# Kernel optimization log

Hardware: AMD Instinct MI355X
Metric: run time of the kernel (lower is better)

The kernel has to match this reference:

```python
import jax, jax.numpy as jnp
import numpy as np

RANK = 16
BN_EPS = 1e-5


def _head(xf, qw, qb, kw, kb, vw, vb, qlw, klw, ow, ob):
    # xf: [B, S, c]  (c = split channels)
    Q = xf @ qw.T + qb
    K = xf @ kw.T + kb
    V = xf @ vw.T + vb
    Ql = Q @ qlw.T                      # [B, S, rank]
    Kl = K @ klw.T                      # [B, S, rank]
    scores = jnp.einsum('bsr,btr->bst', Ql, Kl) / jnp.sqrt(jnp.float32(RANK))
    attn = jax.nn.softmax(scores, axis=-1)   # [B, S, S]
    out = jnp.einsum('bst,btc->bsc', attn, V)
    return out @ ow.T + ob


def _bn(x, g, b):
    # training-mode BatchNorm2d: biased batch stats over (B, H, W)
    m = x.mean(axis=(0, 2, 3), keepdims=True)
    v = x.var(axis=(0, 2, 3), keepdims=True)
    return (x - m) / jnp.sqrt(v + BN_EPS) * g[None, :, None, None] + b[None, :, None, None]


def reference(x, qw, qb, kw, kb, vw, vb, qlw, klw, ow, ob,
              f1w, f1b, f2w, f2b, g1, b1, g2, b2):
    B, C, H, W = x.shape
    sc = C // 4
    S = H * W
    xf = x.reshape(B, C, S).transpose(0, 2, 1)   # [B, S, C]

    outs = []
    prev = jnp.zeros_like(xf[..., :sc])
    for i in range(4):  # hierarchical: head i consumes split_i + out_{i-1}
        xi = xf[..., i * sc:(i + 1) * sc] + prev
        prev = _head(xi, qw[i], qb[i], kw[i], kb[i], vw[i], vb[i],
                     qlw[i], klw[i], ow[i], ob[i])
        outs.append(prev)

    concat = jnp.concatenate(outs, axis=-1).transpose(0, 2, 1).reshape(B, C, H, W)
    out = x + _bn(concat, g1, b1)

    # FFN: 1x1 conv 256->1024, exact GELU, 1x1 conv 1024->256 (dropout = eval / identity)
    h = jnp.einsum('bchw,oc->bohw', out, f1w) + f1b[None, :, None, None]
    h = jax.nn.gelu(h, approximate=False)
    h = jnp.einsum('bchw,oc->bohw', h, f2w) + f2b[None, :, None, None]
    return out + _bn(h, g2, b2)


def setup_inputs() -> dict:
    key = jax.random.key(0)
    ks = jax.random.split(key, 16)
    B, C, H, W = 2, 256, 64, 64
    sc = C // 4
    s = 0.05
    inp = {
        'x':   jax.random.normal(ks[0], (B, C, H, W), jnp.float32),
        'qw':  jax.random.normal(ks[1], (4, sc, sc), jnp.float32) * s,
        'qb':  jnp.zeros((4, sc), jnp.float32),
        'kw':  jax.random.normal(ks[2], (4, sc, sc), jnp.float32) * s,
        'kb':  jnp.zeros((4, sc), jnp.float32),
        'vw':  jax.random.normal(ks[3], (4, sc, sc), jnp.float32) * s,
        'vb':  jnp.zeros((4, sc), jnp.float32),
        'qlw': jax.random.normal(ks[4], (4, RANK, sc), jnp.float32) * s,
        'klw': jax.random.normal(ks[5], (4, RANK, sc), jnp.float32) * s,
        'ow':  jax.random.normal(ks[6], (4, sc, sc), jnp.float32) * s,
        'ob':  jnp.zeros((4, sc), jnp.float32),
        'f1w': jax.random.normal(ks[7], (4 * C, C), jnp.float32) * s,
        'f1b': jnp.zeros((4 * C,), jnp.float32),
        'f2w': jax.random.normal(ks[8], (C, 4 * C), jnp.float32) * s,
        'f2b': jnp.zeros((C,), jnp.float32),
        'g1':  jnp.ones((C,), jnp.float32),
        'b1':  jnp.zeros((C,), jnp.float32),
        'g2':  jnp.ones((C,), jnp.float32),
        'b2':  jnp.zeros((C,), jnp.float32),
    }
    return inp
```

## Files before the change

### kernel.cpp

```cpp
#include <hip/hip_runtime.h>
#include <math.h>

#define SS 4096
#define CC 256
#define NB 2
#define KSPLIT 8
#define KCHUNK (SS / KSPLIT)
#define KT 64
#define QTM 128

typedef __bf16 bf16x8 __attribute__((ext_vector_type(8)));
typedef float f32x4 __attribute__((ext_vector_type(4)));

__device__ inline float b2f(unsigned short u) {
    union { float f; unsigned int i; } x; x.i = ((unsigned int)u) << 16; return x.f;
}

__global__ void prep_weights_kernel(const float* __restrict__ qw, const float* __restrict__ qb,
                                    const float* __restrict__ kw, const float* __restrict__ kb,
                                    const float* __restrict__ vw, const float* __restrict__ vb,
                                    const float* __restrict__ qlw, const float* __restrict__ klw,
                                    __bf16* __restrict__ Wall, float* __restrict__ bias_all)
{
    int i = blockIdx.x;
    int t = threadIdx.x;
    for (int idx = t; idx < 16 * 64; idx += 256) {
        int r = idx >> 6, c = idx & 63;
        float sq = 0.f, sk = 0.f;
        for (int j = 0; j < 64; ++j) {
            sq += qlw[(i * 16 + r) * 64 + j] * qw[(i * 64 + j) * 64 + c];
            sk += klw[(i * 16 + r) * 64 + j] * kw[(i * 64 + j) * 64 + c];
        }
        Wall[i * 6144 + idx] = (__bf16)(0.25f * sq);
        Wall[i * 6144 + 1024 + idx] = (__bf16)sk;
    }
    for (int idx = t; idx < 64 * 64; idx += 256)
        Wall[i * 6144 + 2048 + idx] = (__bf16)vw[i * 4096 + idx];
    if (t < 16) {
        float sq = 0.f, sk = 0.f;
        for (int j = 0; j < 64; ++j) {
            sq += qlw[(i * 16 + t) * 64 + j] * qb[i * 64 + j];
            sk += klw[(i * 16 + t) * 64 + j] * kb[i * 64 + j];
        }
        bias_all[i * 96 + t] = 0.25f * sq;
        bias_all[i * 96 + 16 + t] = sk;
    }
    if (t < 64) bias_all[i * 96 + 32 + t] = vb[i * 64 + t];
}

__global__ void transpose_x_kernel(const float* __restrict__ x, float* __restrict__ xT)
{
    __shared__ float tile[32][33];
    int b = blockIdx.z;
    int s0 = blockIdx.x * 32, c0 = blockIdx.y * 32;
    int tx = threadIdx.x, ty = threadIdx.y;
    const float* xb = x + (size_t)b * CC * SS;
    for (int j = 0; j < 4; ++j)
        tile[ty + 8 * j][tx] = xb[(size_t)(c0 + ty + 8 * j) * SS + s0 + tx];
    __syncthreads();
    float* xTb = xT + (size_t)b * SS * CC;
    for (int j = 0; j < 4; ++j)
        xTb[(size_t)(s0 + ty + 8 * j) * CC + c0 + tx] = tile[tx][ty + 8 * j];
}

__global__ void f32_to_bf16_kernel(const float* __restrict__ src, __bf16* __restrict__ dst, int n)
{
    int i = (blockIdx.x * 256 + threadIdx.x) * 4;
    if (i < n) {
        float4 v = *(const float4*)&src[i];
        union { uint2 u; __bf16 b[4]; } pk;
        pk.b[0] = (__bf16)v.x; pk.b[1] = (__bf16)v.y;
        pk.b[2] = (__bf16)v.z; pk.b[3] = (__bf16)v.w;
        *(uint2*)&dst[i] = pk.u;
    }
}

__global__ __launch_bounds__(256) void head_qkv_mfma_kernel(
    const float* __restrict__ xT, const float* __restrict__ conc,
    const __bf16* __restrict__ Wall, const float* __restrict__ bias_all,
    __bf16* __restrict__ Qlb, __bf16* __restrict__ Klb, __bf16* __restrict__ Vtb, int head)
{
    __shared__ __align__(16) __bf16 sXi[32 * 72];
    __shared__ __align__(16) __bf16 sW[96 * 72];
    __shared__ __align__(16) __bf16 sVtT[64 * 40];
    __shared__ float sBias[96];

    const int t = threadIdx.x;
    const int b = blockIdx.y;
    const int s0 = blockIdx.x * 32;
    const int lane = t & 63, wv = t >> 6;
    const int wm = wv & 1, wnh = wv >> 1;
    const int c = lane & 15, g = lane >> 4;

    #pragma unroll
    for (int i = 0; i < 6; ++i) {
        int e = t + i * 256;
        int row = e >> 4, c4 = (e & 15) * 4;
        *(uint2*)&sW[row * 72 + c4] = *(const uint2*)&Wall[head * 6144 + row * 64 + c4];
    }
    if (t < 96) sBias[t] = bias_all[head * 96 + t];

    #pragma unroll
    for (int i = 0; i < 2; ++i) {
        int idx = t + i * 256;
        int row = idx >> 4, c4 = (idx & 15) * 4;
        size_t grow = (size_t)(b * SS + s0 + row);
        float4 v = *(const float4*)&xT[grow * CC + head * 64 + c4];
        if (head > 0) {
            float4 p = *(const float4*)&conc[grow * CC + (head - 1) * 64 + c4];
            v.x += p.x; v.y += p.y; v.z += p.z; v.w += p.w;
        }
        union { uint2 u; __bf16 bb[4]; } pk;
        pk.bb[0] = (__bf16)v.x; pk.bb[1] = (__bf16)v.y;
        pk.bb[2] = (__bf16)v.z; pk.bb[3] = (__bf16)v.w;
        *(uint2*)&sXi[row * 72 + c4] = pk.u;
    }
    __syncthreads();

    bf16x8 aX0 = *(const bf16x8*)&sXi[(wm * 16 + c) * 72 + g * 8];
    bf16x8 aX1 = *(const bf16x8*)&sXi[(wm * 16 + c) * 72 + 32 + g * 8];

    #pragma unroll
    for (int nt = 0; nt < 3; ++nt) {
        int ntile = wnh * 3 + nt;
        bf16x8 bW0 = *(const bf16x8*)&sW[(ntile * 16 + c) * 72 + g * 8];
        bf16x8 bW1 = *(const bf16x8*)&sW[(ntile * 16 + c) * 72 + 32 + g * 8];
        f32x4 d;
        #pragma unroll
        for (int r = 0; r < 4; ++r) d[r] = 0.f;
        d = __builtin_amdgcn_mfma_f32_16x16x32_bf16(aX0, bW0, d, 0, 0, 0);
        d = __builtin_amdgcn_mfma_f32_16x16x32_bf16(aX1, bW1, d, 0, 0, 0);

        int ch = ntile * 16 + c;
        float bb = sBias[ch];
        int srow_l0 = wm * 16 + g * 4;
        #pragma unroll
        for (int r = 0; r < 4; ++r) {
            float v = d[r] + bb;
            int srow = s0 + srow_l0 + r;
            if (ntile == 0)      Qlb[((size_t)b * SS + srow) * 16 + ch] = (__bf16)v;
            else if (ntile == 1) Klb[((size_t)b * SS + srow) * 16 + (ch - 16)] = (__bf16)v;
            else                 sVtT[(ch - 32) * 40 + srow_l0 + r] = (__bf16)v;
        }
    }
    __syncthreads();

    {
        int ch = t >> 2, chunk = t & 3;
        *(uint4*)&Vtb[((size_t)b * 64 + ch) * SS + s0 + chunk * 8] =
            *(const uint4*)&sVtT[ch * 40 + chunk * 8];
    }
}

__global__ __launch_bounds__(512) void attn_mfma_kernel(
    const __bf16* __restrict__ Qlb, const __bf16* __restrict__ Klb,
    const __bf16* __restrict__ Vtb,
    __bf16* __restrict__ pacc, float* __restrict__ pm, float* __restrict__ pl)
{
    __shared__ __align__(16) __bf16 sK[64 * 24];
    __shared__ __align__(16) __bf16 sVt[64 * 64];
    __shared__ __align__(16) __bf16 sP[8][16 * 64];

    const int t = threadIdx.x;
    const int lane = t & 63, wv = t >> 6;
    const int b = blockIdx.z, chunk = blockIdx.y;
    const int g = lane >> 4, qi = lane & 15;
    const int qrow = blockIdx.x * QTM + wv * 16 + qi;

    bf16x8 bQ;
    #pragma unroll
    for (int j = 0; j < 8; ++j) bQ[j] = (__bf16)0.f;
    if (lane < 32) bQ = *(const bf16x8*)(Qlb + ((size_t)b * SS + qrow) * 16 + g * 8);

    f32x4 acc[4];
    #pragma unroll
    for (int cs = 0; cs < 4; ++cs)
        #pragma unroll
        for (int r = 0; r < 4; ++r) acc[cs][r] = 0.f;
    float mrun = -1e30f, lrun = 0.f;

    __bf16* Pw = &sP[wv][0];
    const size_t kbase = (size_t)b * SS;
    const int kbeg = chunk * KCHUNK;

    for (int kt0 = kbeg; kt0 < kbeg + KCHUNK; kt0 += KT) {
        __syncthreads();
        if (t < 256) {
            int kk = t >> 2, quad = t & 3;
            *(uint2*)((char*)sK + kk * 48 + quad * 8) =
                *(const uint2*)(Klb + (kbase + kt0 + kk) * 16 + quad * 4);
        }
        {
            int c = t >> 3, sl = t & 7;
            int ksrc = (sl ^ (c & 7)) * 8;
            uint4 v = *(const uint4*)(Vtb + ((size_t)b * 64 + c) * SS + kt0 + ksrc);
            *(uint4*)((char*)sVt + c * 128 + sl * 16) = v;
        }
        __syncthreads();

        f32x4 st[4];
        #pragma unroll
        for (int ks = 0; ks < 4; ++ks) {
            bf16x8 aK;
            #pragma unroll
            for (int j = 0; j < 8; ++j) aK[j] = (__bf16)0.f;
            if (lane < 32)
                aK = *(const bf16x8*)((char*)sK + (ks * 16 + qi) * 48 + g * 16);
            f32x4 z;
            #pragma unroll
            for (int r = 0; r < 4; ++r) z[r] = 0.f;
            st[ks] = __builtin_amdgcn_mfma_f32_16x16x32_bf16(aK, bQ, z, 0, 0, 0);
        }

        float tmax = -1e30f;
        #pragma unroll
        for (int ks = 0; ks < 4; ++ks)
            #pragma unroll
            for (int r = 0; r < 4; ++r) tmax = fmaxf(tmax, st[ks][r]);
        tmax = fmaxf(tmax, __shfl_xor(tmax, 16));
        tmax = fmaxf(tmax, __shfl_xor(tmax, 32));
        float mnew = fmaxf(mrun, tmax);
        float scale = __expf(mrun - mnew);
        float psum = 0.f;
        #pragma unroll
        for (int ks = 0; ks < 4; ++ks) {
            union { uint2 u; __bf16 bb[4]; } pk;
            #pragma unroll
            for (int r = 0; r < 4; ++r) {
                float p = __expf(st[ks][r] - mnew);
                psum += p;
                pk.bb[r] = (__bf16)p;
            }
            int off = (qi * 128 + ks * 32 + g * 8) ^ ((qi & 7) << 4);
            *(uint2*)((char*)Pw + off) = pk.u;
        }
        psum += __shfl_xor(psum, 16);
        psum += __shfl_xor(psum, 32);
        lrun = lrun * scale + psum;
        mrun = mnew;
        #pragma unroll
        for (int cs = 0; cs < 4; ++cs) acc[cs] *= scale;

        #pragma unroll
        for (int kc = 0; kc < 2; ++kc) {
            int boff = (qi * 128 + kc * 64 + g * 16) ^ ((qi & 7) << 4);
            bf16x8 bP = *(const bf16x8*)((char*)Pw + boff);
            #pragma unroll
            for (int cs = 0; cs < 4; ++cs) {
                int c = cs * 16 + qi;
                int aoff = (c * 128 + kc * 64 + g * 16) ^ ((c & 7) << 4);
                bf16x8 aV = *(const bf16x8*)((char*)sVt + aoff);
                acc[cs] = __builtin_amdgcn_mfma_f32_16x16x32_bf16(aV, bP, acc[cs], 0, 0, 0);
            }
        }
    }

    size_t prow = (size_t)(b * KSPLIT + chunk) * SS + qrow;
    #pragma unroll
    for (int cs = 0; cs < 4; ++cs) {
        union { uint2 u; __bf16 bb[4]; } pk;
        #pragma unroll
        for (int r = 0; r < 4; ++r) pk.bb[r] = (__bf16)acc[cs][r];
        *(uint2*)(pacc + prow * 64 + cs * 16 + g * 4) = pk.u;
    }
    if (lane < 16) { pm[prow] = mrun; pl[prow] = lrun; }
}

__global__ __launch_bounds__(512) void attn_combine_kernel(
    const __bf16* __restrict__ pacc, const float* __restrict__ pm, const float* __restrict__ pl,
    const float* __restrict__ ow, const float* __restrict__ ob,
    float* __restrict__ conc, float* __restrict__ gsum, float* __restrict__ gss, int head)
{
    __shared__ float sO[32][66];
    __shared__ float sOWt[64][68];
    __shared__ float sob[64];
    __shared__ float lsum[64], lss[64];

    const int t = threadIdx.x;
    const int b = blockIdx.y;
    const int s0 = blockIdx.x * 32;
    const int q = t >> 4;
    const int gk = t & 15;
    const int vc0 = gk * 4;

    if (t < 64) { lsum[t] = 0.f; lss[t] = 0.f; }
    for (int idx = t; idx < 4096; idx += 512) {
        int co = idx >> 6, k = idx & 63;
        sOWt[k][co] = ow[head * 4096 + idx];
    }
    if (t < 64) sob[t] = ob[head * 64 + t];

    float pmv[KSPLIT];
    float mstar = -1e30f;
    #pragma unroll
    for (int c = 0; c < KSPLIT; ++c) {
        pmv[c] = pm[(size_t)(b * KSPLIT + c) * SS + s0 + q];
        mstar = fmaxf(mstar, pmv[c]);
    }
    float l = 0.f;
    float o0 = 0.f, o1 = 0.f, o2 = 0.f, o3 = 0.f;
    const unsigned short* pu = (const unsigned short*)pacc;
    #pragma unroll
    for (int c = 0; c < KSPLIT; ++c) {
        size_t prow = (size_t)(b * KSPLIT + c) * SS + s0 + q;
        float w = __expf(pmv[c] - mstar);
        l += w * pl[prow];
        ushort4 a4 = *(const ushort4*)&pu[prow * 64 + vc0];
        o0 += w * b2f(a4.x); o1 += w * b2f(a4.y); o2 += w * b2f(a4.z); o3 += w * b2f(a4.w);
    }
    float inv_l = 1.f / l;
    sO[q][vc0 + 0] = o0 * inv_l;
    sO[q][vc0 + 1] = o1 * inv_l;
    sO[q][vc0 + 2] = o2 * inv_l;
    sO[q][vc0 + 3] = o3 * inv_l;
    __syncthreads();

    float e[4];
    #pragma unroll
    for (int j = 0; j < 4; ++j) e[j] = sob[vc0 + j];
    #pragma unroll 8
    for (int k = 0; k < 64; ++k) {
        float ov = sO[q][k];
        float4 w4 = *(const float4*)&sOWt[k][vc0];
        e[0] += ov * w4.x; e[1] += ov * w4.y; e[2] += ov * w4.z; e[3] += ov * w4.w;
    }
    float* cp = conc + (size_t)(b * SS + s0 + q) * CC + head * 64 + vc0;
    float4 r; r.x = e[0]; r.y = e[1]; r.z = e[2]; r.w = e[3];
    *(float4*)cp = r;

    float sv[4], sq[4];
    #pragma unroll
    for (int j = 0; j < 4; ++j) { sv[j] = e[j]; sq[j] = e[j] * e[j]; }
    #pragma unroll
    for (int j = 0; j < 4; ++j) {
        sv[j] += __shfl_xor(sv[j], 16); sv[j] += __shfl_xor(sv[j], 32);
        sq[j] += __shfl_xor(sq[j], 16); sq[j] += __shfl_xor(sq[j], 32);
    }
    if ((t & 48) == 0) {
        #pragma unroll
        for (int j = 0; j < 4; ++j) {
            atomicAdd(&lsum[vc0 + j], sv[j]);
            atomicAdd(&lss[vc0 + j], sq[j]);
        }
    }
    __syncthreads();
    if (t < 64) {
        atomicAdd(&gsum[head * 64 + t], lsum[t]);
        atomicAdd(&gss[head * 64 + t], lss[t]);
    }
}

__global__ void bn_apply1_kernel(const float* __restrict__ xT, const float* __restrict__ conc,
                                 const float* __restrict__ sum, const float* __restrict__ sumsq,
                                 const float* __restrict__ g, const float* __restrict__ bta,
                                 __bf16* __restrict__ out1b)
{
    size_t idx = (size_t)blockIdx.x * 256 + threadIdx.x;
    int c = threadIdx.x;
    float mean = sum[c] * (1.f / 8192.f);
    float var = sumsq[c] * (1.f / 8192.f) - mean * mean;
    float rstd = rsqrtf(var + 1e-5f);
    float v = xT[idx] + (conc[idx] - mean) * rstd * g[c] + bta[c];
    out1b[idx] = (__bf16)v;
}

__global__ __launch_bounds__(256) void gemm1_mfma_kernel(
    const __bf16* __restrict__ A, const __bf16* __restrict__ W,
    const float* __restrict__ bias, __bf16* __restrict__ out, int N, int K)
{
    constexpr int MREP = 4;
    constexpr int BM = 2 * MREP * 16;
    __shared__ __align__(16) __bf16 sA[BM * 72];
    __shared__ __align__(16) __bf16 sB[64 * 72];

    const int t = threadIdx.x;
    const int lane = t & 63, wv = t >> 6;
    const int wm = wv & 1, wn = wv >> 1;
    const int g = lane >> 4, c = lane & 15;
    const int m0 = blockIdx.x * BM, n0 = blockIdx.y * 64;

    f32x4 acc[MREP][2];
    #pragma unroll
    for (int mi = 0; mi < MREP; ++mi)
        #pragma unroll
        for (int ni = 0; ni < 2; ++ni)
            #pragma unroll
            for (int r = 0; r < 4; ++r) acc[mi][ni][r] = 0.f;

    const int rS = t >> 3, ksS = (t & 7) * 8;

    for (int k0 = 0; k0 < K; k0 += 64) {
        __syncthreads();
        #pragma unroll
        for (int i = 0; i < MREP; ++i) {
            int r = rS + i * 32;
            *(uint4*)&sA[r * 72 + ksS] = *(const uint4*)&A[(size_t)(m0 + r) * K + k0 + ksS];
        }
        #pragma unroll
        for (int i = 0; i < 2; ++i) {
            int r = rS + i * 32;
            *(uint4*)&sB[r * 72 + ksS] = *(const uint4*)&W[(size_t)(n0 + r) * K + k0 + ksS];
        }
        __syncthreads();

        #pragma unroll
        for (int kk = 0; kk < 2; ++kk) {
            bf16x8 bfr[2];
            #pragma unroll
            for (int ni = 0; ni < 2; ++ni)
                bfr[ni] = *(const bf16x8*)&sB[(wn * 32 + ni * 16 + c) * 72 + kk * 32 + g * 8];
            #pragma unroll
            for (int mi = 0; mi < MREP; ++mi) {
                bf16x8 afr = *(const bf16x8*)&sA[(wm * MREP * 16 + mi * 16 + c) * 72 + kk * 32 + g * 8];
                #pragma unroll
                for (int ni = 0; ni < 2; ++ni)
                    acc[mi][ni] = __builtin_amdgcn_mfma_f32_16x16x32_bf16(afr, bfr[ni], acc[mi][ni], 0, 0, 0);
            }
        }
    }

    #pragma unroll
    for (int ni = 0; ni < 2; ++ni) {
        int col = n0 + wn * 32 + ni * 16 + c;
        float bb = bias[col];
        #pragma unroll
        for (int mi = 0; mi < MREP; ++mi) {
            int row0 = m0 + wm * MREP * 16 + mi * 16 + g * 4;
            #pragma unroll
            for (int r = 0; r < 4; ++r) {
                float v = acc[mi][ni][r] + bb;
                v = 0.5f * v * (1.f + erff(v * 0.70710678118654752f));
                out[(size_t)(row0 + r) * N + col] = (__bf16)v;
            }
        }
    }
}

__global__ __launch_bounds__(256) void gemm2_mfma_stats_kernel(
    const __bf16* __restrict__ A, const __bf16* __restrict__ W,
    const float* __restrict__ bias, __bf16* __restrict__ out,
    float* __restrict__ gsum, float* __restrict__ gss, int N, int K)
{
    constexpr int MREP = 2;
    constexpr int BM = 2 * MREP * 16;
    __shared__ __align__(16) __bf16 sA[BM * 72];
    __shared__ __align__(16) __bf16 sB[64 * 72];
    __shared__ float lsum[64], lss[64];

    const int t = threadIdx.x;
    const int lane = t & 63, wv = t >> 6;
    const int wm = wv & 1, wn = wv >> 1;
    const int g = lane >> 4, c = lane & 15;
    const int m0 = blockIdx.x * BM, n0 = blockIdx.y * 64;

    if (t < 64) { lsum[t] = 0.f; lss[t] = 0.f; }

    f32x4 acc[MREP][2];
    #pragma unroll
    for (int mi = 0; mi < MREP; ++mi)
        #pragma unroll
        for (int ni = 0; ni < 2; ++ni)
            #pragma unroll
            for (int r = 0; r < 4; ++r) acc[mi][ni][r] = 0.f;

    const int rS = t >> 3, ksS = (t & 7) * 8;

    for (int k0 = 0; k0 < K; k0 += 64) {
        __syncthreads();
        #pragma unroll
        for (int i = 0; i < MREP; ++i) {
            int r = rS + i * 32;
            *(uint4*)&sA[r * 72 + ksS] = *(const uint4*)&A[(size_t)(m0 + r) * K + k0 + ksS];
        }
        #pragma unroll
        for (int i = 0; i < 2; ++i) {
            int r = rS + i * 32;
            *(uint4*)&sB[r * 72 + ksS] = *(const uint4*)&W[(size_t)(n0 + r) * K + k0 + ksS];
        }
        __syncthreads();

        #pragma unroll
        for (int kk = 0; kk < 2; ++kk) {
            bf16x8 bfr[2];
            #pragma unroll
            for (int ni = 0; ni < 2; ++ni)
                bfr[ni] = *(const bf16x8*)&sB[(wn * 32 + ni * 16 + c) * 72 + kk * 32 + g * 8];
            #pragma unroll
            for (int mi = 0; mi < MREP; ++mi) {
                bf16x8 afr = *(const bf16x8*)&sA[(wm * MREP * 16 + mi * 16 + c) * 72 + kk * 32 + g * 8];
                #pragma unroll
                for (int ni = 0; ni < 2; ++ni)
                    acc[mi][ni] = __builtin_amdgcn_mfma_f32_16x16x32_bf16(afr, bfr[ni], acc[mi][ni], 0, 0, 0);
            }
        }
    }

    #pragma unroll
    for (int ni = 0; ni < 2; ++ni) {
        int col = n0 + wn * 32 + ni * 16 + c;
        float bb = bias[col];
        float ps = 0.f, pss = 0.f;
        #pragma unroll
        for (int mi = 0; mi < MREP; ++mi) {
            int row0 = m0 + wm * MREP * 16 + mi * 16 + g * 4;
            #pragma unroll
            for (int r = 0; r < 4; ++r) {
                float v = acc[mi][ni][r] + bb;
                out[(size_t)(row0 + r) * N + col] = (__bf16)v;
                ps += v; pss += v * v;
            }
        }
        ps += __shfl_xor(ps, 16); ps += __shfl_xor(ps, 32);
        pss += __shfl_xor(pss, 16); pss += __shfl_xor(pss, 32);
        if ((t & 48) == 0) {
            atomicAdd(&lsum[wn * 32 + ni * 16 + c], ps);
            atomicAdd(&lss[wn * 32 + ni * 16 + c], pss);
        }
    }
    __syncthreads();
    if (t < 64) {
        atomicAdd(&gsum[n0 + t], lsum[t]);
        atomicAdd(&gss[n0 + t], lss[t]);
    }
}

__global__ void bn_final_kernel(const __bf16* __restrict__ out1b, const __bf16* __restrict__ h2b,
                                const float* __restrict__ sum, const float* __restrict__ sumsq,
                                const float* __restrict__ g, const float* __restrict__ bta,
                                float* __restrict__ out)
{
    __shared__ float tile[32][33];
    int b = blockIdx.z;
    int s0 = blockIdx.x * 32, c0 = blockIdx.y * 32;
    int tx = threadIdx.x, ty = threadIdx.y;
    const unsigned short* o1 = (const unsigned short*)out1b;
    const unsigned short* h2 = (const unsigned short*)h2b;
    for (int j = 0; j < 4; ++j) {
        int c = c0 + tx;
        int s = s0 + ty + 8 * j;
        size_t idx = ((size_t)b * SS + s) * CC + c;
        float mean = sum[c] * (1.f / 8192.f);
        float var = sumsq[c] * (1.f / 8192.f) - mean * mean;
        float rstd = rsqrtf(var + 1e-5f);
        tile[ty + 8 * j][tx] = b2f(o1[idx]) + (b2f(h2[idx]) - mean) * rstd * g[c] + bta[c];
    }
    __syncthreads();
    for (int j = 0; j < 4; ++j) {
        int c = c0 + ty + 8 * j;
        int s = s0 + tx;
        out[((size_t)b * CC + c) * SS + s] = tile[tx][ty + 8 * j];
    }
}

extern "C" void kernel_launch(void* const* d_in, const int* in_sizes, int n_in,
                              void* d_out, int out_size, void* d_ws, size_t ws_size,
                              hipStream_t stream)
{
    const float* x   = (const float*)d_in[0];
    const float* qw  = (const float*)d_in[1];
    const float* qb  = (const float*)d_in[2];
    const float* kw  = (const float*)d_in[3];
    const float* kb  = (const float*)d_in[4];
    const float* vw  = (const float*)d_in[5];
    const float* vb  = (const float*)d_in[6];
    const float* qlw = (const float*)d_in[7];
    const float* klw = (const float*)d_in[8];
    const float* ow  = (const float*)d_in[9];
    const float* ob  = (const float*)d_in[10];
    const float* f1w = (const float*)d_in[11];
    const float* f1b = (const float*)d_in[12];
    const float* f2w = (const float*)d_in[13];
    const float* f2b = (const float*)d_in[14];
    const float* g1  = (const float*)d_in[15];
    const float* b1  = (const float*)d_in[16];
    const float* g2  = (const float*)d_in[17];
    const float* b2  = (const float*)d_in[18];
    float* outp = (float*)d_out;

    float* ws = (float*)d_ws;
    size_t off = 0;
    float* xT    = ws + off; off += (size_t)NB * SS * CC;
    float* conc  = ws + off; off += (size_t)NB * SS * CC;
    float* Hreg  = ws + off; off += (size_t)NB * SS * 1024 / 2;
    __bf16* out1b = (__bf16*)(ws + off); off += (size_t)NB * SS * CC / 2;
    __bf16* h2b   = (__bf16*)(ws + off); off += (size_t)NB * SS * CC / 2;
    __bf16* Qlb  = (__bf16*)(ws + off); off += (size_t)NB * SS * 16 / 2;
    __bf16* Klb  = (__bf16*)(ws + off); off += (size_t)NB * SS * 16 / 2;
    __bf16* Vtb  = (__bf16*)(ws + off); off += (size_t)NB * 64 * SS / 2;
    __bf16* f1wb = (__bf16*)(ws + off); off += (size_t)1024 * CC / 2;
    __bf16* f2wb = (__bf16*)(ws + off); off += (size_t)CC * 1024 / 2;
    __bf16* Wall = (__bf16*)(ws + off); off += 4 * 6144 / 2;
    float* bias_all = ws + off; off += 4 * 96;
    float* stats = ws + off; off += 1024;
    float* sum1 = stats, *sumsq1 = stats + 256, *sum2 = stats + 512, *sumsq2 = stats + 768;

    __bf16* pacc = (__bf16*)Hreg;
    float* pm = Hreg + (size_t)NB * KSPLIT * SS * 64 / 2;
    float* pl = pm + (size_t)NB * KSPLIT * SS;
    __bf16* h1b = (__bf16*)Hreg;

    hipMemsetAsync(stats, 0, 1024 * sizeof(float), stream);

    prep_weights_kernel<<<4, 256, 0, stream>>>(qw, qb, kw, kb, vw, vb, qlw, klw, Wall, bias_all);
    transpose_x_kernel<<<dim3(SS / 32, CC / 32, NB), dim3(32, 8), 0, stream>>>(x, xT);
    f32_to_bf16_kernel<<<(1024 * CC) / 1024, 256, 0, stream>>>(f1w, f1wb, 1024 * CC);
    f32_to_bf16_kernel<<<(CC * 1024) / 1024, 256, 0, stream>>>(f2w, f2wb, CC * 1024);

    for (int head = 0; head < 4; ++head) {
        head_qkv_mfma_kernel<<<dim3(SS / 32, NB), 256, 0, stream>>>(
            xT, conc, Wall, bias_all, Qlb, Klb, Vtb, head);
        attn_mfma_kernel<<<dim3(SS / QTM, KSPLIT, NB), 512, 0, stream>>>(
            Qlb, Klb, Vtb, pacc, pm, pl);
        attn_combine_kernel<<<dim3(SS / 32, NB), 512, 0, stream>>>(
            pacc, pm, pl, ow, ob, conc, sum1, sumsq1, head);
    }

    bn_apply1_kernel<<<(NB * SS * CC) / 256, 256, 0, stream>>>(
        xT, conc, sum1, sumsq1, g1, b1, out1b);

    gemm1_mfma_kernel<<<dim3((NB * SS) / 128, 1024 / 64), 256, 0, stream>>>(
        out1b, f1wb, f1b, h1b, 1024, CC);
    gemm2_mfma_stats_kernel<<<dim3((NB * SS) / 64, CC / 64), 256, 0, stream>>>(
        h1b, f2wb, f2b, h2b, sum2, sumsq2, CC, 1024);

    bn_final_kernel<<<dim3(SS / 32, CC / 32, NB), dim3(32, 8), 0, stream>>>(
        out1b, h2b, sum2, sumsq2, g2, b2, outp);
}
```

Baseline: 322.7 us.

## Fuse next-head QKV projection into combine kernel and prefetch attention tiles

```diff
diff --git a/kernel.cpp b/kernel.cpp
--- a/kernel.cpp
+++ b/kernel.cpp
@@ -16,12 +16,15 @@
     union { float f; unsigned int i; } x; x.i = ((unsigned int)u) << 16; return x.f;
 }
 
+__device__ inline float fast_exp2(float x) { return __builtin_amdgcn_exp2f(x); }
+
 __global__ void prep_weights_kernel(const float* __restrict__ qw, const float* __restrict__ qb,
                                     const float* __restrict__ kw, const float* __restrict__ kb,
                                     const float* __restrict__ vw, const float* __restrict__ vb,
                                     const float* __restrict__ qlw, const float* __restrict__ klw,
                                     __bf16* __restrict__ Wall, float* __restrict__ bias_all)
 {
+    const float QSC = 0.25f * 1.44269504088896340736f;
     int i = blockIdx.x;
     int t = threadIdx.x;
     for (int idx = t; idx < 16 * 64; idx += 256) {
@@ -31,7 +34,7 @@
             sq += qlw[(i * 16 + r) * 64 + j] * qw[(i * 64 + j) * 64 + c];
             sk += klw[(i * 16 + r) * 64 + j] * kw[(i * 64 + j) * 64 + c];
         }
-        Wall[i * 6144 + idx] = (__bf16)(0.25f * sq);
+        Wall[i * 6144 + idx] = (__bf16)(QSC * sq);
         Wall[i * 6144 + 1024 + idx] = (__bf16)sk;
     }
     for (int idx = t; idx < 64 * 64; idx += 256)
@@ -42,7 +45,7 @@
             sq += qlw[(i * 16 + t) * 64 + j] * qb[i * 64 + j];
             sk += klw[(i * 16 + t) * 64 + j] * kb[i * 64 + j];
         }
-        bias_all[i * 96 + t] = 0.25f * sq;
+        bias_all[i * 96 + t] = QSC * sq;
         bias_all[i * 96 + 16 + t] = sk;
     }
     if (t < 64) bias_all[i * 96 + 32 + t] = vb[i * 64 + t];
@@ -144,7 +147,6 @@
         }
     }
     __syncthreads();
-
     {
         int ch = t >> 2, chunk = t & 3;
         *(uint4*)&Vtb[((size_t)b * 64 + ch) * SS + s0 + chunk * 8] =
@@ -182,23 +184,29 @@
     __bf16* Pw = &sP[wv][0];
     const size_t kbase = (size_t)b * SS;
     const int kbeg = chunk * KCHUNK;
-
-    for (int kt0 = kbeg; kt0 < kbeg + KCHUNK; kt0 += KT) {
-        __syncthreads();
-        if (t < 256) {
-            int kk = t >> 2, quad = t & 3;
-            *(uint2*)((char*)sK + kk * 48 + quad * 8) =
-                *(const uint2*)(Klb + (kbase + kt0 + kk) * 16 + quad * 4);
-        }
-        {
-            int c = t >> 3, sl = t & 7;
-            int ksrc = (sl ^ (c & 7)) * 8;
-            uint4 v = *(const uint4*)(Vtb + ((size_t)b * 64 + c) * SS + kt0 + ksrc);
-            *(uint4*)((char*)sVt + c * 128 + sl * 16) = v;
-        }
-        __syncthreads();
+    const int kend = kbeg + KCHUNK;
+
+    const int skk = t >> 2, squad = t & 3;
+    const int svc = t >> 3, svsl = t & 7;
+    const int svksrc = (svsl ^ (svc & 7)) * 8;
+
+    uint2 rK;
+    uint4 rV;
+    if (t < 256) rK = *(const uint2*)(Klb + (kbase + kbeg + skk) * 16 + squad * 4);
+    rV = *(const uint4*)(Vtb + ((size_t)b * 64 + svc) * SS + kbeg + svksrc);
+    if (t < 256) *(uint2*)((char*)sK + skk * 48 + squad * 8) = rK;
+    *(uint4*)((char*)sVt + svc * 128 + svsl * 16) = rV;
+    __syncthreads();
+
+    for (int kt0 = kbeg; kt0 < kend; kt0 += KT) {
+        const bool more = (kt0 + KT) < kend;
+        if (more) {
+            if (t < 256) rK = *(const uint2*)(Klb + (kbase + kt0 + KT + skk) * 16 + squad * 4);
+            rV = *(const uint4*)(Vtb + ((size_t)b * 64 + svc) * SS + kt0 + KT + svksrc);
+        }
 
         f32x4 st[4];
+        __builtin_amdgcn_s_setprio(1);
         #pragma unroll
         for (int ks = 0; ks < 4; ++ks) {
             bf16x8 aK;
@@ -211,6 +219,7 @@
             for (int r = 0; r < 4; ++r) z[r] = 0.f;
             st[ks] = __builtin_amdgcn_mfma_f32_16x16x32_bf16(aK, bQ, z, 0, 0, 0);
         }
+        __builtin_amdgcn_s_setprio(0);
 
         float tmax = -1e30f;
         #pragma unroll
@@ -220,14 +229,14 @@
         tmax = fmaxf(tmax, __shfl_xor(tmax, 16));
         tmax = fmaxf(tmax, __shfl_xor(tmax, 32));
         float mnew = fmaxf(mrun, tmax);
-        float scale = __expf(mrun - mnew);
+        float scale = fast_exp2(mrun - mnew);
         float psum = 0.f;
         #pragma unroll
         for (int ks = 0; ks < 4; ++ks) {
             union { uint2 u; __bf16 bb[4]; } pk;
             #pragma unroll
             for (int r = 0; r < 4; ++r) {
-                float p = __expf(st[ks][r] - mnew);
+                float p = fast_exp2(st[ks][r] - mnew);
                 psum += p;
                 pk.bb[r] = (__bf16)p;
             }
@@ -241,6 +250,7 @@
         #pragma unroll
         for (int cs = 0; cs < 4; ++cs) acc[cs] *= scale;
 
+        __builtin_amdgcn_s_setprio(1);
         #pragma unroll
         for (int kc = 0; kc < 2; ++kc) {
             int boff = (qi * 128 + kc * 64 + g * 16) ^ ((qi & 7) << 4);
@@ -253,6 +263,14 @@
                 acc[cs] = __builtin_amdgcn_mfma_f32_16x16x32_bf16(aV, bP, acc[cs], 0, 0, 0);
             }
         }
+        __builtin_amdgcn_s_setprio(0);
+
+        if (more) {
+            __syncthreads();
+            if (t < 256) *(uint2*)((char*)sK + skk * 48 + squad * 8) = rK;
+            *(uint4*)((char*)sVt + svc * 128 + svsl * 16) = rV;
+            __syncthreads();
+        }
     }
 
     size_t prow = (size_t)(b * KSPLIT + chunk) * SS + qrow;
@@ -266,15 +284,22 @@
     if (lane < 16) { pm[prow] = mrun; pl[prow] = lrun; }
 }
 
-__global__ __launch_bounds__(512) void attn_combine_kernel(
+__global__ __launch_bounds__(512) void combine_qkv_kernel(
     const __bf16* __restrict__ pacc, const float* __restrict__ pm, const float* __restrict__ pl,
     const float* __restrict__ ow, const float* __restrict__ ob,
-    float* __restrict__ conc, float* __restrict__ gsum, float* __restrict__ gss, int head)
+    const float* __restrict__ xT, const __bf16* __restrict__ Wall,
+    const float* __restrict__ bias_all,
+    float* __restrict__ conc, float* __restrict__ gsum, float* __restrict__ gss,
+    __bf16* __restrict__ Qlb, __bf16* __restrict__ Klb, __bf16* __restrict__ Vtb, int head)
 {
     __shared__ float sO[32][66];
     __shared__ float sOWt[64][68];
     __shared__ float sob[64];
     __shared__ float lsum[64], lss[64];
+    __shared__ __align__(16) __bf16 sXi[32 * 72];
+    __shared__ __align__(16) __bf16 sW[96 * 72];
+    __shared__ __align__(16) __bf16 sVtT[64 * 40];
+    __shared__ float sBias[96];
 
     const int t = threadIdx.x;
     const int b = blockIdx.y;
@@ -282,6 +307,7 @@
     const int q = t >> 4;
     const int gk = t & 15;
     const int vc0 = gk * 4;
+    const int nexth = head + 1;
 
     if (t < 64) { lsum[t] = 0.f; lss[t] = 0.f; }
     for (int idx = t; idx < 4096; idx += 512) {
@@ -289,6 +315,15 @@
         sOWt[k][co] = ow[head * 4096 + idx];
     }
     if (t < 64) sob[t] = ob[head * 64 + t];
+    if (head < 3) {
+        #pragma unroll
+        for (int i = 0; i < 3; ++i) {
+            int e = t + i * 512;
+            int row = e >> 4, c4 = (e & 15) * 4;
+            *(uint2*)&sW[row * 72 + c4] = *(const uint2*)&Wall[nexth * 6144 + row * 64 + c4];
+        }
+        if (t < 96) sBias[t] = bias_all[nexth * 96 + t];
+    }
 
     float pmv[KSPLIT];
     float mstar = -1e30f;
@@ -303,7 +338,7 @@
     #pragma unroll
     for (int c = 0; c < KSPLIT; ++c) {
         size_t prow = (size_t)(b * KSPLIT + c) * SS + s0 + q;
-        float w = __expf(pmv[c] - mstar);
+        float w = fast_exp2(pmv[c] - mstar);
         l += w * pl[prow];
         ushort4 a4 = *(const ushort4*)&pu[prow * 64 + vc0];
         o0 += w * b2f(a4.x); o1 += w * b2f(a4.y); o2 += w * b2f(a4.z); o3 += w * b2f(a4.w);
@@ -328,25 +363,76 @@
     float4 r; r.x = e[0]; r.y = e[1]; r.z = e[2]; r.w = e[3];
     *(float4*)cp = r;
 
-    float sv[4], sq[4];
-    #pragma unroll
-    for (int j = 0; j < 4; ++j) { sv[j] = e[j]; sq[j] = e[j] * e[j]; }
+    float sv[4], sq2[4];
+    #pragma unroll
+    for (int j = 0; j < 4; ++j) { sv[j] = e[j]; sq2[j] = e[j] * e[j]; }
     #pragma unroll
     for (int j = 0; j < 4; ++j) {
         sv[j] += __shfl_xor(sv[j], 16); sv[j] += __shfl_xor(sv[j], 32);
-        sq[j] += __shfl_xor(sq[j], 16); sq[j] += __shfl_xor(sq[j], 32);
+        sq2[j] += __shfl_xor(sq2[j], 16); sq2[j] += __shfl_xor(sq2[j], 32);
     }
     if ((t & 48) == 0) {
         #pragma unroll
         for (int j = 0; j < 4; ++j) {
             atomicAdd(&lsum[vc0 + j], sv[j]);
-            atomicAdd(&lss[vc0 + j], sq[j]);
-        }
+            atomicAdd(&lss[vc0 + j], sq2[j]);
+        }
+    }
+
+    if (head < 3) {
+        size_t grow = (size_t)(b * SS + s0 + q);
+        float4 xv = *(const float4*)&xT[grow * CC + nexth * 64 + vc0];
+        union { uint2 u; __bf16 bb[4]; } pk;
+        pk.bb[0] = (__bf16)(xv.x + e[0]);
+        pk.bb[1] = (__bf16)(xv.y + e[1]);
+        pk.bb[2] = (__bf16)(xv.z + e[2]);
+        pk.bb[3] = (__bf16)(xv.w + e[3]);
+        *(uint2*)&sXi[q * 72 + vc0] = pk.u;
     }
     __syncthreads();
+
     if (t < 64) {
         atomicAdd(&gsum[head * 64 + t], lsum[t]);
         atomicAdd(&gss[head * 64 + t], lss[t]);
+    }
+
+    if (head < 3) {
+        const int lane = t & 63, wv = t >> 6;
+        const int wm = wv & 1, wn = wv >> 1;
+        const int c = lane & 15, g = lane >> 4;
+
+        bf16x8 aX0 = *(const bf16x8*)&sXi[(wm * 16 + c) * 72 + g * 8];
+        bf16x8 aX1 = *(const bf16x8*)&sXi[(wm * 16 + c) * 72 + 32 + g * 8];
+
+        #pragma unroll
+        for (int ni = 0; ni < 2; ++ni) {
+            int ntile = wn + ni * 4;
+            if (ntile < 6) {
+                bf16x8 bW0 = *(const bf16x8*)&sW[(ntile * 16 + c) * 72 + g * 8];
+                bf16x8 bW1 = *(const bf16x8*)&sW[(ntile * 16 + c) * 72 + 32 + g * 8];
+                f32x4 d;
+                #pragma unroll
+                for (int r = 0; r < 4; ++r) d[r] = 0.f;
+                d = __builtin_amdgcn_mfma_f32_16x16x32_bf16(aX0, bW0, d, 0, 0, 0);
+                d = __builtin_amdgcn_mfma_f32_16x16x32_bf16(aX1, bW1, d, 0, 0, 0);
+
+                int ch = ntile * 16 + c;
+                float bb = sBias[ch];
+                int srow_l0 = wm * 16 + g * 4;
+                #pragma unroll
+                for (int r = 0; r < 4; ++r) {
+                    float v = d[r] + bb;
+                    int srow = s0 + srow_l0 + r;
+                    if (ntile == 0)      Qlb[((size_t)b * SS + srow) * 16 + ch] = (__bf16)v;
+                    else if (ntile == 1) Klb[((size_t)b * SS + srow) * 16 + (ch - 16)] = (__bf16)v;
+                    else                 sVtT[(ch - 32) * 40 + srow_l0 + r] = (__bf16)v;
+                }
+            }
+        }
+        __syncthreads();
+        int ch = t >> 3, chunk = t & 7;
+        *(uint2*)&Vtb[((size_t)b * 64 + ch) * SS + s0 + chunk * 4] =
+            *(const uint2*)&sVtT[ch * 40 + chunk * 4];
     }
 }
 
@@ -599,20 +685,21 @@
     float* pl = pm + (size_t)NB * KSPLIT * SS;
     __bf16* h1b = (__bf16*)Hreg;
 
-    hipMemsetAsync(stats, 0, 1024 * sizeof(float), stream);
+    (void)hipMemsetAsync(stats, 0, 1024 * sizeof(float), stream);
 
     prep_weights_kernel<<<4, 256, 0, stream>>>(qw, qb, kw, kb, vw, vb, qlw, klw, Wall, bias_all);
     transpose_x_kernel<<<dim3(SS / 32, CC / 32, NB), dim3(32, 8), 0, stream>>>(x, xT);
     f32_to_bf16_kernel<<<(1024 * CC) / 1024, 256, 0, stream>>>(f1w, f1wb, 1024 * CC);
     f32_to_bf16_kernel<<<(CC * 1024) / 1024, 256, 0, stream>>>(f2w, f2wb, CC * 1024);
 
+    head_qkv_mfma_kernel<<<dim3(SS / 32, NB), 256, 0, stream>>>(
+        xT, conc, Wall, bias_all, Qlb, Klb, Vtb, 0);
     for (int head = 0; head < 4; ++head) {
-        head_qkv_mfma_kernel<<<dim3(SS / 32, NB), 256, 0, stream>>>(
-            xT, conc, Wall, bias_all, Qlb, Klb, Vtb, head);
         attn_mfma_kernel<<<dim3(SS / QTM, KSPLIT, NB), 512, 0, stream>>>(
             Qlb, Klb, Vtb, pacc, pm, pl);
-        attn_combine_kernel<<<dim3(SS / 32, NB), 512, 0, stream>>>(
-            pacc, pm, pl, ow, ob, conc, sum1, sumsq1, head);
+        combine_qkv_kernel<<<dim3(SS / 32, NB), 512, 0, stream>>>(
+            pacc, pm, pl, ow, ob, xT, Wall, bias_all,
+            conc, sum1, sumsq1, Qlb, Klb, Vtb, head);
     }
 
     bn_apply1_kernel<<<(NB * SS * CC) / 256, 256, 0, stream>>>(
```

Measured after the change: 300.8 us. 6.8% less time.
